# Kernel optimization log

Measured on AMD Instinct MI355X. Metric: run time of the kernel, lower is better.

The kernel has to match this reference:

```python
import jax, jax.numpy as jnp
import numpy as np

N_EMBD = 768
N_HEAD = 12
HEAD_DIM = N_EMBD // N_HEAD
B, S = 2, 2048


def setup_inputs() -> dict:
    key = jax.random.key(0)
    k1, k2, k3 = jax.random.split(key, 3)
    scale = 0.02
    return {
        "hidden_states": jax.random.normal(k1, (B, S, N_EMBD), dtype=jnp.float32),
        "w_attn": jax.random.normal(k2, (N_EMBD, 3 * N_EMBD), dtype=jnp.float32) * scale,
        "b_attn": jnp.zeros((3 * N_EMBD,), dtype=jnp.float32),
        "w_proj": jax.random.normal(k3, (N_EMBD, N_EMBD), dtype=jnp.float32) * scale,
        "b_proj": jnp.zeros((N_EMBD,), dtype=jnp.float32),
    }


def reference(hidden_states, w_attn, b_attn, w_proj, b_proj):
    b, s, d = hidden_states.shape
    qkv = hidden_states @ w_attn + b_attn  # [B,S,3D]
    q, k, v = jnp.split(qkv, 3, axis=-1)
    # split heads: [B,S,D] -> [B,H,S,hd]
    def split_heads(t):
        return t.reshape(b, s, N_HEAD, HEAD_DIM).transpose(0, 2, 1, 3)
    q, k, v = split_heads(q), split_heads(k), split_heads(v)
    scores = jnp.einsum("bhqd,bhkd->bhqk", q, k) / jnp.sqrt(jnp.float32(HEAD_DIM))
    # causal mask: strict upper triangle -> -inf
    mask = jnp.triu(jnp.ones((s, s), dtype=bool), k=1)
    scores = jnp.where(mask, -jnp.inf, scores)
    attn = jax.nn.softmax(scores, axis=-1)
    out = jnp.einsum("bhqk,bhkd->bhqd", attn, v)  # [B,H,S,hd]
    out = out.transpose(0, 2, 1, 3).reshape(b, s, d)  # merge heads
    return out @ w_proj + b_proj
```

## Files before the change

kernel.cpp:

```cpp
#include <hip/hip_runtime.h>
#include <hip/hip_bf16.h>

#define BATCH 2
#define SEQ   2048
#define DMODEL 768
#define NHEAD 12
#define HDIM  64
#define QKVD  2304

typedef __bf16 bf16x8 __attribute__((ext_vector_type(8)));
typedef float f32x4 __attribute__((ext_vector_type(4)));
typedef float f32x16 __attribute__((ext_vector_type(16)));

static __device__ inline f32x4 mfma16(bf16x8 a, bf16x8 b, f32x4 c) {
    return __builtin_amdgcn_mfma_f32_16x16x32_bf16(a, b, c, 0, 0, 0);
}
static __device__ inline f32x16 mfma32(bf16x8 a, bf16x8 b, f32x16 c) {
    return __builtin_amdgcn_mfma_f32_32x32x16_bf16(a, b, c, 0, 0, 0);
}

static __device__ inline unsigned short f2bf_bits(float f) {
    __hip_bfloat16 h = __float2bfloat16(f);
    return __builtin_bit_cast(unsigned short, h);
}
static __device__ inline unsigned int pack_bf16(float a, float b) {
    return (unsigned int)f2bf_bits(a) | ((unsigned int)f2bf_bits(b) << 16);
}

static __device__ inline void gload16(const __hip_bfloat16* g, __hip_bfloat16* l) {
    __builtin_amdgcn_global_load_lds(
        (const __attribute__((address_space(1))) void*)g,
        (__attribute__((address_space(3))) void*)l, 16, 0, 0);
}


__global__ __launch_bounds__(256) void f32_to_bf16_k(const float* __restrict__ in,
                                                     __hip_bfloat16* __restrict__ out) {
    int i = blockIdx.x * 256 + threadIdx.x;
    float4 v = reinterpret_cast<const float4*>(in)[i];
    ushort4 o;
    o.x = f2bf_bits(v.x); o.y = f2bf_bits(v.y);
    o.z = f2bf_bits(v.z); o.w = f2bf_bits(v.w);
    reinterpret_cast<ushort4*>(out)[i] = o;
}

__global__ __launch_bounds__(256) void transpose_f32_to_bf16(const float* __restrict__ in,
                                                             __hip_bfloat16* __restrict__ out,
                                                             int R, int C) {
    __shared__ float t[32][33];
    int tx = threadIdx.x & 31, ty = threadIdx.x >> 5;
    int bx = blockIdx.x * 32;
    int by = blockIdx.y * 32;
#pragma unroll
    for (int k = 0; k < 4; k++)
        t[ty + k * 8][tx] = in[(size_t)(by + ty + k * 8) * C + bx + tx];
    __syncthreads();
#pragma unroll
    for (int k = 0; k < 4; k++)
        out[(size_t)(bx + ty + k * 8) * R + by + tx] = __float2bfloat16(t[tx][ty + k * 8]);
}


__global__ __launch_bounds__(256) void gemm_qkv(const __hip_bfloat16* __restrict__ A,
                                                const __hip_bfloat16* __restrict__ Bt,
                                                const float* __restrict__ bias,
                                                __hip_bfloat16* __restrict__ Qp,
                                                __hip_bfloat16* __restrict__ Kp,
                                                __hip_bfloat16* __restrict__ Vp,
                                                int M, int N, int K) {
    __shared__ __hip_bfloat16 Al[2][128 * 32];
    __shared__ __hip_bfloat16 Bl[2][128 * 32];

    int tid = threadIdx.x;
    int wid = tid >> 6;
    int lane = tid & 63;
    int lr = lane & 15;
    int lg = lane >> 4;
    int m0 = blockIdx.y * 128;
    int n0 = blockIdx.x * 128;
    int wm = (wid >> 1) * 64;
    int wn = (wid & 1) * 64;

    int srow = wid * 16 + (lane >> 2);
    int scol = (lane & 3) * 8;
    const __hip_bfloat16* ag = A + (size_t)(m0 + srow) * K + scol;
    const __hip_bfloat16* bg = Bt + (size_t)(n0 + srow) * K + scol;
    int lofs = wid * 512;

    f32x4 acc[4][4] = {};

    gload16(ag, &Al[0][lofs]);
    gload16(ag + (size_t)64 * K, &Al[0][lofs + 2048]);
    gload16(bg, &Bl[0][lofs]);
    gload16(bg + (size_t)64 * K, &Bl[0][lofs + 2048]);
    __syncthreads();

    int nk = K >> 5;
    for (int t = 0; t < nk; t++) {
        int cb = t & 1;
        if (t + 1 < nk) {
            int k0 = (t + 1) << 5;
            int nb = cb ^ 1;
            gload16(ag + k0, &Al[nb][lofs]);
            gload16(ag + (size_t)64 * K + k0, &Al[nb][lofs + 2048]);
            gload16(bg + k0, &Bl[nb][lofs]);
            gload16(bg + (size_t)64 * K + k0, &Bl[nb][lofs + 2048]);
        }

        bf16x8 af[4], bfr[4];
#pragma unroll
        for (int i = 0; i < 4; i++)
            af[i] = *reinterpret_cast<const bf16x8*>(&Al[cb][(wm + i * 16 + lr) * 32 + lg * 8]);
#pragma unroll
        for (int j = 0; j < 4; j++)
            bfr[j] = *reinterpret_cast<const bf16x8*>(&Bl[cb][(wn + j * 16 + lr) * 32 + lg * 8]);
#pragma unroll
        for (int i = 0; i < 4; i++)
#pragma unroll
            for (int j = 0; j < 4; j++)
                acc[i][j] = mfma16(af[i], bfr[j], acc[i][j]);
        __syncthreads();
    }

#pragma unroll
    for (int j = 0; j < 4; j++) {
        int col = n0 + wn + j * 16 + lr;
        float bv = bias[col];
        int reg = col / DMODEL;
        int cm = col - reg * DMODEL;
        int h = cm >> 6;
        int dd = cm & 63;
        __hip_bfloat16* dstQK = (reg == 0) ? Qp : Kp;
        if (reg < 2) {
            int kd = dd >> 4, half = (dd >> 3) & 1, e = dd & 7;
            int tbase = (kd * 2 + half) * 32;
#pragma unroll
            for (int i = 0; i < 4; i++) {
#pragma unroll
                for (int r = 0; r < 4; r++) {
                    int row = m0 + wm + i * 16 + lg * 4 + r;
                    int bq = row >> 11, tok = row & 2047;
                    size_t off = (size_t)(bq * NHEAD + h) * 131072 + (size_t)(tok >> 5) * 2048
                               + (size_t)(tbase + (tok & 31)) * 8 + e;
                    dstQK[off] = __float2bfloat16(acc[i][j][r] + bv);
                }
            }
        } else {
            int dh = dd >> 5, l31v = dd & 31;
#pragma unroll
            for (int i = 0; i < 4; i++) {
                int row0 = m0 + wm + i * 16 + lg * 4;
                int bq = row0 >> 11, tok0 = row0 & 2047;
                int ks = (tok0 >> 4) & 1, half = (tok0 >> 3) & 1;
                size_t off = (size_t)(bq * NHEAD + h) * 131072 + (size_t)(tok0 >> 5) * 2048
                           + (size_t)((((ks * 2 + dh) * 2 + half) * 32) + l31v) * 8 + (tok0 & 7);
                ushort4 w4;
                w4.x = f2bf_bits(acc[i][j][0] + bv);
                w4.y = f2bf_bits(acc[i][j][1] + bv);
                w4.z = f2bf_bits(acc[i][j][2] + bv);
                w4.w = f2bf_bits(acc[i][j][3] + bv);
                *reinterpret_cast<ushort4*>(Vp + off) = w4;
            }
        }
    }
}


template <bool OUT_BF16>
__global__ __launch_bounds__(256) void gemm_bt(const __hip_bfloat16* __restrict__ A,
                                               const __hip_bfloat16* __restrict__ Bt,
                                               const float* __restrict__ bias,
                                               void* __restrict__ Cp,
                                               int M, int N, int K, int lda) {
    __shared__ __hip_bfloat16 Al[2][128 * 32];
    __shared__ __hip_bfloat16 Bl[2][128 * 32];

    int tid = threadIdx.x;
    int wid = tid >> 6;
    int lane = tid & 63;
    int lr = lane & 15;
    int lg = lane >> 4;
    int m0 = blockIdx.y * 128;
    int n0 = blockIdx.x * 128;
    int wm = (wid >> 1) * 64;
    int wn = (wid & 1) * 64;

    int srow = wid * 16 + (lane >> 2);
    int scol = (lane & 3) * 8;
    const __hip_bfloat16* ag = A + (size_t)(m0 + srow) * lda + scol;
    const __hip_bfloat16* bg = Bt + (size_t)(n0 + srow) * K + scol;
    int lofs = wid * 512;

    f32x4 acc[4][4] = {};

    gload16(ag, &Al[0][lofs]);
    gload16(ag + (size_t)64 * lda, &Al[0][lofs + 2048]);
    gload16(bg, &Bl[0][lofs]);
    gload16(bg + (size_t)64 * K, &Bl[0][lofs + 2048]);
    __syncthreads();

    int nk = K >> 5;
    for (int t = 0; t < nk; t++) {
        int cb = t & 1;
        if (t + 1 < nk) {
            int k0 = (t + 1) << 5;
            int nb = cb ^ 1;
            gload16(ag + k0, &Al[nb][lofs]);
            gload16(ag + (size_t)64 * lda + k0, &Al[nb][lofs + 2048]);
            gload16(bg + k0, &Bl[nb][lofs]);
            gload16(bg + (size_t)64 * K + k0, &Bl[nb][lofs + 2048]);
        }

        bf16x8 af[4], bfr[4];
#pragma unroll
        for (int i = 0; i < 4; i++)
            af[i] = *reinterpret_cast<const bf16x8*>(&Al[cb][(wm + i * 16 + lr) * 32 + lg * 8]);
#pragma unroll
        for (int j = 0; j < 4; j++)
            bfr[j] = *reinterpret_cast<const bf16x8*>(&Bl[cb][(wn + j * 16 + lr) * 32 + lg * 8]);
#pragma unroll
        for (int i = 0; i < 4; i++)
#pragma unroll
            for (int j = 0; j < 4; j++)
                acc[i][j] = mfma16(af[i], bfr[j], acc[i][j]);
        __syncthreads();
    }

#pragma unroll
    for (int i = 0; i < 4; i++) {
#pragma unroll
        for (int j = 0; j < 4; j++) {
            int col = n0 + wn + j * 16 + lr;
            float bv = bias[col];
#pragma unroll
            for (int r = 0; r < 4; r++) {
                int row = m0 + wm + i * 16 + lg * 4 + r;
                float v = acc[i][j][r] + bv;
                if (OUT_BF16)
                    ((__hip_bfloat16*)Cp)[(size_t)row * N + col] = __float2bfloat16(v);
                else
                    ((float*)Cp)[(size_t)row * N + col] = v;
            }
        }
    }
}


#define KS2 0.18033688f

__global__ __launch_bounds__(256, 4) void flash_attn(const __hip_bfloat16* __restrict__ Qp,
                                                     const __hip_bfloat16* __restrict__ Kp,
                                                     const __hip_bfloat16* __restrict__ Vp,
                                                     __hip_bfloat16* __restrict__ AO) {
    __shared__ __align__(16) char smem[30208];

    int tid = threadIdx.x;
    int w = tid >> 6;
    int lane = tid & 63;
    int l31 = lane & 31;
    int lg2 = lane >> 5;

    int wg = blockIdx.x;
    int xcd = wg & 7;
    int slot = wg >> 3;
    int hsl = slot % 3;
    int qsl = slot / 3;
    int bh = xcd * 3 + hsl;
    int it = 63 - qsl;
    int b = bh / NHEAD;
    int h = bh - b * NHEAD;
    int q0 = it * 32;
    int bbase = b * SEQ;

    int Tw = (it >= w) ? ((it - w) >> 2) + 1 : 0;

    const __hip_bfloat16* Kph = Kp + (size_t)bh * 131072;
    const __hip_bfloat16* Vph = Vp + (size_t)bh * 131072;

    bf16x8 qf[4];
    {
        const __hip_bfloat16* qr = Qp + (size_t)bh * 131072 + (size_t)it * 2048 + l31 * 8;
#pragma unroll
        for (int kd = 0; kd < 4; kd++)
            qf[kd] = *reinterpret_cast<const bf16x8*>(qr + (kd * 2 + lg2) * 256);
    }

    f32x16 o0 = {}, o1 = {};
    float m = -3.0e38f, l = 0.f;

    bf16x8 kc[4];
    {
        const __hip_bfloat16* kr = Kph + (size_t)w * 2048 + l31 * 8;
#pragma unroll
        for (int kd = 0; kd < 4; kd++)
            kc[kd] = *reinterpret_cast<const bf16x8*>(kr + (kd * 2 + lg2) * 256);
    }

    for (int t = 0; t < Tw; t++) {
        int qi = 4 * t + w;
        int kvbase = qi * 32;
        bool hn = (t + 1 < Tw);

        const __hip_bfloat16* vr = Vph + (size_t)qi * 2048 + lg2 * 256 + l31 * 8;
        bf16x8 vf[4];
#pragma unroll
        for (int ks = 0; ks < 2; ks++)
#pragma unroll
            for (int dh = 0; dh < 2; dh++)
                vf[ks * 2 + dh] = *reinterpret_cast<const bf16x8*>(vr + (ks * 2 + dh) * 512);

        __builtin_amdgcn_s_setprio(1);
        f32x16 st = {};
#pragma unroll
        for (int kd = 0; kd < 4; kd++)
            st = mfma32(kc[kd], qf[kd], st);
        __builtin_amdgcn_s_setprio(0);

        if (hn) {
            const __hip_bfloat16* kr = Kph + (size_t)(qi + 4) * 2048 + l31 * 8;
#pragma unroll
            for (int kd = 0; kd < 4; kd++)
                kc[kd] = *reinterpret_cast<const bf16x8*>(kr + (kd * 2 + lg2) * 256);
        }

        if (kvbase == q0) {
#pragma unroll
            for (int j = 0; j < 16; j++) {
                int kvl = (j & 3) + 8 * (j >> 2) + 4 * lg2;
                if (kvl > l31) st[j] = -3.0e38f;
            }
        }
        float tm[16];
#pragma unroll
        for (int j = 0; j < 16; j++) tm[j] = st[j];
#pragma unroll
        for (int dd = 8; dd >= 1; dd >>= 1)
#pragma unroll
            for (int j = 0; j < 8; j++)
                if (j < dd) tm[j] = fmaxf(tm[j], tm[j + dd]);
        float mx = fmaxf(tm[0], __shfl_xor(tm[0], 32, 64));
        bool small = __all(mx <= m + 44.0f);
        float mnew = small ? m : fmaxf(m, mx);
#pragma unroll
        for (int j = 0; j < 16; j++)
            st[j] = __builtin_amdgcn_exp2f((st[j] - mnew) * KS2);
        float ts[16];
#pragma unroll
        for (int j = 0; j < 16; j++) ts[j] = st[j];
#pragma unroll
        for (int dd = 8; dd >= 1; dd >>= 1)
#pragma unroll
            for (int j = 0; j < 8; j++)
                if (j < dd) ts[j] += ts[j + dd];
        float ls = ts[0] + __shfl_xor(ts[0], 32, 64);
        if (small) {
            l += ls;
        } else {
            float sc = __builtin_amdgcn_exp2f((m - mnew) * KS2);
            l = l * sc + ls;
            o0 *= sc;
            o1 *= sc;
            m = mnew;
        }

#pragma unroll
        for (int ks = 0; ks < 2; ks++) {
            unsigned int a0 = pack_bf16(st[8 * ks + 0], st[8 * ks + 1]);
            unsigned int a1 = pack_bf16(st[8 * ks + 2], st[8 * ks + 3]);
            unsigned int b0 = pack_bf16(st[8 * ks + 4], st[8 * ks + 5]);
            unsigned int b1 = pack_bf16(st[8 * ks + 6], st[8 * ks + 7]);
            unsigned int y0 = lg2 ? a0 : b0;
            unsigned int y1 = lg2 ? a1 : b1;
            unsigned int p0 = __shfl_xor(y0, 32, 64);
            unsigned int p1 = __shfl_xor(y1, 32, 64);
            union { unsigned int u[4]; bf16x8 v; } pf;
            pf.u[0] = lg2 ? p0 : a0;
            pf.u[1] = lg2 ? p1 : a1;
            pf.u[2] = lg2 ? b0 : p0;
            pf.u[3] = lg2 ? b1 : p1;
            __builtin_amdgcn_s_setprio(1);
            o0 = mfma32(vf[ks * 2 + 0], pf.v, o0);
            o1 = mfma32(vf[ks * 2 + 1], pf.v, o1);
            __builtin_amdgcn_s_setprio(0);
        }
    }

    __syncthreads();

    if (w != 0) {
        float* SCw = (float*)(smem + (w - 1) * 8448);
#pragma unroll
        for (int j = 0; j < 16; j++) {
            int dl = (j & 3) + 8 * (j >> 2) + 4 * lg2;
            SCw[dl * 32 + l31] = o0[j];
            SCw[(32 + dl) * 32 + l31] = o1[j];
        }
        if (lg2 == 0) {
            SCw[2048 + l31] = m;
            SCw[2048 + 32 + l31] = l;
        }
    }
    __syncthreads();
    if (w == 0) {
        float* SC1 = (float*)(smem + 0);
        float* SC2 = (float*)(smem + 8448);
        float* SC3 = (float*)(smem + 16896);
        __hip_bfloat16* OL = (__hip_bfloat16*)(smem + 25344);
        float m1 = SC1[2048 + l31], l1 = SC1[2048 + 32 + l31];
        float m2 = SC2[2048 + l31], l2 = SC2[2048 + 32 + l31];
        float m3 = SC3[2048 + l31], l3 = SC3[2048 + 32 + l31];
        float M = fmaxf(fmaxf(m, m1), fmaxf(m2, m3));
        float e0 = __builtin_amdgcn_exp2f((m - M) * KS2);
        float e1 = __builtin_amdgcn_exp2f((m1 - M) * KS2);
        float e2 = __builtin_amdgcn_exp2f((m2 - M) * KS2);
        float e3 = __builtin_amdgcn_exp2f((m3 - M) * KS2);
        float L = l * e0 + l1 * e1 + l2 * e2 + l3 * e3;
        float linv = 1.0f / L;
#pragma unroll
        for (int od = 0; od < 2; od++) {
#pragma unroll
            for (int g = 0; g < 4; g++) {
                int dbase = od * 32 + 8 * g + 4 * lg2;
                ushort4 w4;
#pragma unroll
                for (int r = 0; r < 4; r++) {
                    int d = dbase + r;
                    float self = od ? o1[4 * g + r] : o0[4 * g + r];
                    float v = self * e0 + SC1[d * 32 + l31] * e1 +
                              SC2[d * 32 + l31] * e2 + SC3[d * 32 + l31] * e3;
                    v *= linv;
                    ((unsigned short*)&w4)[r] = f2bf_bits(v);
                }
                *reinterpret_cast<ushort4*>(&OL[l31 * 72 + dbase]) = w4;
            }
        }
    }
    __syncthreads();
    {
        __hip_bfloat16* OL = (__hip_bfloat16*)(smem + 25344);
        int r = tid >> 3, c = (tid & 7) * 8;
        __hip_bfloat16* dst = AO + (size_t)(bbase + q0 + r) * DMODEL + h * HDIM + c;
        *reinterpret_cast<uint4*>(dst) = *reinterpret_cast<const uint4*>(&OL[r * 72 + c]);
    }
}


extern "C" void kernel_launch(void* const* d_in, const int* in_sizes, int n_in,
                              void* d_out, int out_size, void* d_ws, size_t ws_size,
                              hipStream_t stream) {
    const float* hidden = (const float*)d_in[0];
    const float* w_attn = (const float*)d_in[1];
    const float* b_attn = (const float*)d_in[2];
    const float* w_proj = (const float*)d_in[3];
    const float* b_proj = (const float*)d_in[4];
    float* out = (float*)d_out;

    char* ws = (char*)d_ws;
    __hip_bfloat16* Xb  = (__hip_bfloat16*)(ws + 0);
    __hip_bfloat16* Wta = (__hip_bfloat16*)(ws + 6291456);
    __hip_bfloat16* Wtp = (__hip_bfloat16*)(ws + 9830400);
    __hip_bfloat16* Qpb = (__hip_bfloat16*)(ws + 11010048);
    __hip_bfloat16* Kpb = (__hip_bfloat16*)(ws + 17301504);
    __hip_bfloat16* Vpb = (__hip_bfloat16*)(ws + 23592960);
    __hip_bfloat16* AO  = (__hip_bfloat16*)(ws + 29884416);

    const int M = BATCH * SEQ;

    f32_to_bf16_k<<<dim3(M * DMODEL / (256 * 4)), dim3(256), 0, stream>>>(hidden, Xb);
    transpose_f32_to_bf16<<<dim3(QKVD / 32, DMODEL / 32), dim3(256), 0, stream>>>(w_attn, Wta, DMODEL, QKVD);
    transpose_f32_to_bf16<<<dim3(DMODEL / 32, DMODEL / 32), dim3(256), 0, stream>>>(w_proj, Wtp, DMODEL, DMODEL);
    gemm_qkv<<<dim3(QKVD / 128, M / 128), dim3(256), 0, stream>>>(Xb, Wta, b_attn, Qpb, Kpb, Vpb, M, QKVD, DMODEL);
    flash_attn<<<dim3(1536), dim3(256), 0, stream>>>(Qpb, Kpb, Vpb, AO);
    gemm_bt<false><<<dim3(DMODEL / 128, M / 128), dim3(256), 0, stream>>>(AO, Wtp, b_proj, out, M, DMODEL, DMODEL, DMODEL);
}
```

Baseline: 88.33 us.

## Software-pipeline QK^T MFMA ahead of softmax and fuse prep kernels

The flash-attention inner loop now computes the next tile's QK^T scores before issuing the current tile's PV MFMAs. The goal is to overlap matrix work with the softmax and exp math, and the K prefetch now runs two tiles ahead. The three input-conversion and transpose kernels are merged into one launch that dispatches on block index, which removes two kernel launches. In exchange the loop holds more live registers (an extra score accumulator), which may lower occupancy.

```diff
diff --git a/kernel.cpp b/kernel.cpp
--- a/kernel.cpp
+++ b/kernel.cpp
@@ -34,23 +34,36 @@
 }
 
 
-__global__ __launch_bounds__(256) void f32_to_bf16_k(const float* __restrict__ in,
-                                                     __hip_bfloat16* __restrict__ out) {
-    int i = blockIdx.x * 256 + threadIdx.x;
-    float4 v = reinterpret_cast<const float4*>(in)[i];
-    ushort4 o;
-    o.x = f2bf_bits(v.x); o.y = f2bf_bits(v.y);
-    o.z = f2bf_bits(v.z); o.w = f2bf_bits(v.w);
-    reinterpret_cast<ushort4*>(out)[i] = o;
-}
-
-__global__ __launch_bounds__(256) void transpose_f32_to_bf16(const float* __restrict__ in,
-                                                             __hip_bfloat16* __restrict__ out,
-                                                             int R, int C) {
+__global__ __launch_bounds__(256) void prep_fused(const float* __restrict__ hidden,
+                                                  __hip_bfloat16* __restrict__ Xb,
+                                                  const float* __restrict__ w_attn,
+                                                  __hip_bfloat16* __restrict__ Wta,
+                                                  const float* __restrict__ w_proj,
+                                                  __hip_bfloat16* __restrict__ Wtp) {
     __shared__ float t[32][33];
+    int blk = blockIdx.x;
+    if (blk < 3072) {
+        int i = blk * 256 + threadIdx.x;
+        float4 v = reinterpret_cast<const float4*>(hidden)[i];
+        ushort4 o;
+        o.x = f2bf_bits(v.x); o.y = f2bf_bits(v.y);
+        o.z = f2bf_bits(v.z); o.w = f2bf_bits(v.w);
+        reinterpret_cast<ushort4*>(Xb)[i] = o;
+        return;
+    }
+    const float* in;
+    __hip_bfloat16* out;
+    int R, C, bx, by;
+    if (blk < 4800) {
+        int k = blk - 3072;
+        in = w_attn; out = Wta; R = DMODEL; C = QKVD;
+        bx = (k % 72) * 32; by = (k / 72) * 32;
+    } else {
+        int k = blk - 4800;
+        in = w_proj; out = Wtp; R = DMODEL; C = DMODEL;
+        bx = (k % 24) * 32; by = (k / 24) * 32;
+    }
     int tx = threadIdx.x & 31, ty = threadIdx.x >> 5;
-    int bx = blockIdx.x * 32;
-    int by = blockIdx.y * 32;
 #pragma unroll
     for (int k = 0; k < 4; k++)
         t[ty + k * 8][tx] = in[(size_t)(by + ty + k * 8) * C + bx + tx];
@@ -289,17 +302,31 @@
     float m = -3.0e38f, l = 0.f;
 
     bf16x8 kc[4];
-    {
+    f32x16 st;
+
+    if (Tw > 0) {
         const __hip_bfloat16* kr = Kph + (size_t)w * 2048 + l31 * 8;
 #pragma unroll
         for (int kd = 0; kd < 4; kd++)
             kc[kd] = *reinterpret_cast<const bf16x8*>(kr + (kd * 2 + lg2) * 256);
+        __builtin_amdgcn_s_setprio(1);
+        f32x16 s = {};
+#pragma unroll
+        for (int kd = 0; kd < 4; kd++)
+            s = mfma32(kc[kd], qf[kd], s);
+        __builtin_amdgcn_s_setprio(0);
+        st = s;
+        if (Tw > 1) {
+            const __hip_bfloat16* kr2 = Kph + (size_t)(w + 4) * 2048 + l31 * 8;
+#pragma unroll
+            for (int kd = 0; kd < 4; kd++)
+                kc[kd] = *reinterpret_cast<const bf16x8*>(kr2 + (kd * 2 + lg2) * 256);
+        }
     }
 
     for (int t = 0; t < Tw; t++) {
         int qi = 4 * t + w;
         int kvbase = qi * 32;
-        bool hn = (t + 1 < Tw);
 
         const __hip_bfloat16* vr = Vph + (size_t)qi * 2048 + lg2 * 256 + l31 * 8;
         bf16x8 vf[4];
@@ -308,20 +335,6 @@
 #pragma unroll
             for (int dh = 0; dh < 2; dh++)
                 vf[ks * 2 + dh] = *reinterpret_cast<const bf16x8*>(vr + (ks * 2 + dh) * 512);
-
-        __builtin_amdgcn_s_setprio(1);
-        f32x16 st = {};
-#pragma unroll
-        for (int kd = 0; kd < 4; kd++)
-            st = mfma32(kc[kd], qf[kd], st);
-        __builtin_amdgcn_s_setprio(0);
-
-        if (hn) {
-            const __hip_bfloat16* kr = Kph + (size_t)(qi + 4) * 2048 + l31 * 8;
-#pragma unroll
-            for (int kd = 0; kd < 4; kd++)
-                kc[kd] = *reinterpret_cast<const bf16x8*>(kr + (kd * 2 + lg2) * 256);
-        }
 
         if (kvbase == q0) {
 #pragma unroll
@@ -363,26 +376,59 @@
             m = mnew;
         }
 
-#pragma unroll
-        for (int ks = 0; ks < 2; ks++) {
-            unsigned int a0 = pack_bf16(st[8 * ks + 0], st[8 * ks + 1]);
-            unsigned int a1 = pack_bf16(st[8 * ks + 2], st[8 * ks + 3]);
-            unsigned int b0 = pack_bf16(st[8 * ks + 4], st[8 * ks + 5]);
-            unsigned int b1 = pack_bf16(st[8 * ks + 6], st[8 * ks + 7]);
+        union PF { unsigned int u[4]; bf16x8 v; };
+        PF pfA, pfB;
+        {
+            unsigned int a0 = pack_bf16(st[0], st[1]);
+            unsigned int a1 = pack_bf16(st[2], st[3]);
+            unsigned int b0 = pack_bf16(st[4], st[5]);
+            unsigned int b1 = pack_bf16(st[6], st[7]);
             unsigned int y0 = lg2 ? a0 : b0;
             unsigned int y1 = lg2 ? a1 : b1;
             unsigned int p0 = __shfl_xor(y0, 32, 64);
             unsigned int p1 = __shfl_xor(y1, 32, 64);
-            union { unsigned int u[4]; bf16x8 v; } pf;
-            pf.u[0] = lg2 ? p0 : a0;
-            pf.u[1] = lg2 ? p1 : a1;
-            pf.u[2] = lg2 ? b0 : p0;
-            pf.u[3] = lg2 ? b1 : p1;
+            pfA.u[0] = lg2 ? p0 : a0;
+            pfA.u[1] = lg2 ? p1 : a1;
+            pfA.u[2] = lg2 ? b0 : p0;
+            pfA.u[3] = lg2 ? b1 : p1;
+        }
+        {
+            unsigned int a0 = pack_bf16(st[8], st[9]);
+            unsigned int a1 = pack_bf16(st[10], st[11]);
+            unsigned int b0 = pack_bf16(st[12], st[13]);
+            unsigned int b1 = pack_bf16(st[14], st[15]);
+            unsigned int y0 = lg2 ? a0 : b0;
+            unsigned int y1 = lg2 ? a1 : b1;
+            unsigned int p0 = __shfl_xor(y0, 32, 64);
+            unsigned int p1 = __shfl_xor(y1, 32, 64);
+            pfB.u[0] = lg2 ? p0 : a0;
+            pfB.u[1] = lg2 ? p1 : a1;
+            pfB.u[2] = lg2 ? b0 : p0;
+            pfB.u[3] = lg2 ? b1 : p1;
+        }
+
+        if (t + 1 < Tw) {
             __builtin_amdgcn_s_setprio(1);
-            o0 = mfma32(vf[ks * 2 + 0], pf.v, o0);
-            o1 = mfma32(vf[ks * 2 + 1], pf.v, o1);
+            f32x16 s = {};
+#pragma unroll
+            for (int kd = 0; kd < 4; kd++)
+                s = mfma32(kc[kd], qf[kd], s);
             __builtin_amdgcn_s_setprio(0);
-        }
+            st = s;
+            if (t + 2 < Tw) {
+                const __hip_bfloat16* kr = Kph + (size_t)(qi + 8) * 2048 + l31 * 8;
+#pragma unroll
+                for (int kd = 0; kd < 4; kd++)
+                    kc[kd] = *reinterpret_cast<const bf16x8*>(kr + (kd * 2 + lg2) * 256);
+            }
+        }
+
+        __builtin_amdgcn_s_setprio(1);
+        o0 = mfma32(vf[0], pfA.v, o0);
+        o1 = mfma32(vf[1], pfA.v, o1);
+        o0 = mfma32(vf[2], pfB.v, o0);
+        o1 = mfma32(vf[3], pfB.v, o1);
+        __builtin_amdgcn_s_setprio(0);
     }
 
     __syncthreads();
@@ -466,9 +512,7 @@
 
     const int M = BATCH * SEQ;
 
-    f32_to_bf16_k<<<dim3(M * DMODEL / (256 * 4)), dim3(256), 0, stream>>>(hidden, Xb);
-    transpose_f32_to_bf16<<<dim3(QKVD / 32, DMODEL / 32), dim3(256), 0, stream>>>(w_attn, Wta, DMODEL, QKVD);
-    transpose_f32_to_bf16<<<dim3(DMODEL / 32, DMODEL / 32), dim3(256), 0, stream>>>(w_proj, Wtp, DMODEL, DMODEL);
+    prep_fused<<<dim3(5376), dim3(256), 0, stream>>>(hidden, Xb, w_attn, Wta, w_proj, Wtp);
     gemm_qkv<<<dim3(QKVD / 128, M / 128), dim3(256), 0, stream>>>(Xb, Wta, b_attn, Qpb, Kpb, Vpb, M, QKVD, DMODEL);
     flash_attn<<<dim3(1536), dim3(256), 0, stream>>>(Qpb, Kpb, Vpb, AO);
     gemm_bt<false><<<dim3(DMODEL / 128, M / 128), dim3(256), 0, stream>>>(AO, Wtp, b_proj, out, M, DMODEL, DMODEL, DMODEL);
```

New measurement: 86.71 us. No clear change (-1.8%).
